# Kernel tuning notes

Hardware: AMD Instinct MI355X
Metric: run time of the kernel (lower is better)

Reference implementation:

```python
import jax, jax.numpy as jnp
import numpy as np

DIM = 2048
NUM_HEADS = 16
HEAD_DIM = DIM // NUM_HEADS
EPS = 1e-6


def rms_norm(x, w, eps=EPS):
    # x: [B, L, C] float; normalize in fp32 semantics
    xf = x.astype(jnp.float32)
    n = xf * jax.lax.rsqrt(jnp.mean(xf * xf, axis=-1, keepdims=True) + eps)
    return n.astype(x.dtype) * w


def rope_apply(x, freqs):
    # x: [B, S, N, D], freqs: [S, D//2]; interleaved rotary in fp32
    xf = x.astype(jnp.float32)
    cos = jnp.cos(freqs).astype(jnp.float32)  # [S, D/2]
    sin = jnp.sin(freqs).astype(jnp.float32)
    B, S, N, D = x.shape
    x2 = xf.reshape(B, S, N, D // 2, 2)
    x_even = x2[..., 0]  # [B,S,N,D/2]
    x_odd = x2[..., 1]
    c = cos[None, :, None, :]
    s = sin[None, :, None, :]
    r_even = x_even * c - x_odd * s
    r_odd = x_even * s + x_odd * c
    out = jnp.stack([r_even, r_odd], axis=-1).reshape(B, S, N, D)
    return out.astype(x.dtype)


def attention(q, k, v):
    # q,k,v: [B, S, N, D] -> [B, S, N, D], standard scaled dot-product
    scale = 1.0 / jnp.sqrt(jnp.asarray(q.shape[-1], q.dtype))
    scores = jnp.einsum('bqnd,bknd->bnqk', q, k) * scale
    p = jax.nn.softmax(scores, axis=-1)
    return jnp.einsum('bnqk,bknd->bqnd', p, v)


def setup_inputs() -> dict:
    key = jax.random.key(0)
    ks = jax.random.split(key, 10)
    B, S = 2, 4096
    x = jax.random.normal(ks[0], (B, S, DIM), dtype=jnp.float32)
    seq_lens = jnp.full((B,), S, dtype=jnp.int32)
    freqs = jax.random.normal(ks[1], (S, HEAD_DIM // 2), dtype=jnp.float32)
    std = 1.0 / np.sqrt(DIM)
    wq = jax.random.normal(ks[2], (DIM, DIM), dtype=jnp.float32) * std
    wk = jax.random.normal(ks[3], (DIM, DIM), dtype=jnp.float32) * std
    wv = jax.random.normal(ks[4], (DIM, DIM), dtype=jnp.float32) * std
    wo = jax.random.normal(ks[5], (DIM, DIM), dtype=jnp.float32) * std
    bq = jnp.zeros((DIM,), jnp.float32)
    bk = jnp.zeros((DIM,), jnp.float32)
    bv = jnp.zeros((DIM,), jnp.float32)
    bo = jnp.zeros((DIM,), jnp.float32)
    gq = jnp.ones((DIM,), jnp.float32)
    gk = jnp.ones((DIM,), jnp.float32)
    return {
        'x': x, 'seq_lens': seq_lens, 'freqs': freqs,
        'wq': wq, 'bq': bq, 'wk': wk, 'bk': bk, 'wv': wv, 'bv': bv,
        'wo': wo, 'bo': bo, 'gq': gq, 'gk': gk,
    }


def reference(x, seq_lens, freqs, wq, bq, wk, bk, wv, bv, wo, bo, gq, gk):
    B, S, C = x.shape
    N, D = NUM_HEADS, HEAD_DIM
    q = rms_norm(x @ wq.T + bq, gq).reshape(B, S, N, D)
    k = rms_norm(x @ wk.T + bk, gk).reshape(B, S, N, D)
    v = (x @ wv.T + bv).reshape(B, S, N, D)
    q = rope_apply(q, freqs)
    k = rope_apply(k, freqs)
    o = attention(q, k, v).reshape(B, S, C)
    return o @ wo.T + bo
```

## Files before the change

kernel.cpp:

```cpp
#include <hip/hip_runtime.h>
#include <hip/hip_bf16.h>

typedef unsigned short u16;
typedef __bf16 bf16x8 __attribute__((ext_vector_type(8)));
typedef float f32x4 __attribute__((ext_vector_type(4)));
typedef float f32x16 __attribute__((ext_vector_type(16)));

#define DIMC  2048
#define NH    16
#define HD    128
#define BSZ   2
#define SEQ   4096
#define MTOK  (BSZ*SEQ)

#define SCALE_L2E (0.08838834764831845f * 1.4426950408889634f)

__device__ __forceinline__ u16 f2bf(float f) {
  unsigned u = __float_as_uint(f);
  u += 0x7fff + ((u >> 16) & 1);
  return (u16)(u >> 16);
}
__device__ __forceinline__ float bf2f(u16 b) {
  return __uint_as_float(((unsigned)b) << 16);
}

__device__ __forceinline__ void gload_lds16(const void* g, void* l) {
  __builtin_amdgcn_global_load_lds(
      (const __attribute__((address_space(1))) void*)g,
      (__attribute__((address_space(3))) void*)l, 16, 0, 0);
}

#define BAR() __builtin_amdgcn_s_barrier()
#define ASM_VMCNT(n) do { asm volatile("s_waitcnt vmcnt(" #n ")" ::: "memory"); \
                          __builtin_amdgcn_sched_barrier(0); } while (0)
#define ASM_LGK0()   do { asm volatile("s_waitcnt lgkmcnt(0)" ::: "memory");    \
                          __builtin_amdgcn_sched_barrier(0); } while (0)

__global__ __launch_bounds__(256) void cast_bf16_k(const float* __restrict__ in,
                                                   u16* __restrict__ out, int n) {
  int i = (blockIdx.x * 256 + threadIdx.x) * 4;
  if (i >= n) return;
  float4 v = *(const float4*)(in + i);
  ushort4 o;
  o.x = f2bf(v.x); o.y = f2bf(v.y); o.z = f2bf(v.z); o.w = f2bf(v.w);
  *(ushort4*)(out + i) = o;
}

__global__ __launch_bounds__(256) void cast_w4_k(
    const float* __restrict__ w0, const float* __restrict__ w1,
    const float* __restrict__ w2, const float* __restrict__ w3,
    u16* __restrict__ out, int n) {
  const int z = blockIdx.z;
  const float* src = (z == 0) ? w0 : (z == 1) ? w1 : (z == 2) ? w2 : w3;
  u16* dst = out + (size_t)z * n;
  int i = (blockIdx.x * 256 + threadIdx.x) * 4;
  if (i >= n) return;
  float4 v = *(const float4*)(src + i);
  ushort4 o;
  o.x = f2bf(v.x); o.y = f2bf(v.y); o.z = f2bf(v.z); o.w = f2bf(v.w);
  *(ushort4*)(dst + i) = o;
}

#define AsBuf(d, h) (SMEM[(d) * 2 + (h)])
#define BsBuf(d, h) (SMEM[4 + (d) * 2 + (h)])

#define STG_A(d, kt, h)                                                        \
  { const u16* s_ = Ag + (size_t)(h) * khalf + (size_t)(kt) * 64;              \
    gload_lds16(s_ + at0, (u16*)AsBuf(d, h) + tid * 8);                        \
    gload_lds16(s_ + at1, (u16*)AsBuf(d, h) + (tid + 512) * 8); }
#define STG_B(d, kt, h)                                                        \
  { const u16* s_ = Bg + (size_t)(h) * khalf + (size_t)(kt) * 64;              \
    gload_lds16(s_ + at0, (u16*)BsBuf(d, h) + tid * 8);                        \
    gload_lds16(s_ + at1, (u16*)BsBuf(d, h) + (tid + 512) * 8); }

#define GPHASE(bb, q, STAGE_CODE, TAIL_CODE)                                   \
  {                                                                            \
    if ((q) == 0) {                                                            \
      _Pragma("unroll") for (int fc = 0; fc < 4; fc++)                         \
        _Pragma("unroll") for (int ks = 0; ks < 2; ks++)                       \
          bfr[fc][ks] = *(const bf16x8*)((const char*)BsBuf(bb, wc >> 1) +     \
              rbB + fc * 2048 + colr[ks]);                                     \
    }                                                                          \
    _Pragma("unroll") for (int e = 0; e < 2; e++)                              \
      _Pragma("unroll") for (int ks = 0; ks < 2; ks++)                         \
        afr[e][ks] = *(const bf16x8*)((const char*)AsBuf(bb, wr) +             \
            rbA + (2 * (q) + e) * 2048 + colr[ks]);                            \
    STAGE_CODE;                                                                \
    BAR();                                                                     \
    ASM_LGK0();                                                                \
    __builtin_amdgcn_s_setprio(1);                                             \
    _Pragma("unroll") for (int e = 0; e < 2; e++)                              \
      _Pragma("unroll") for (int fc = 0; fc < 4; fc++)                         \
        _Pragma("unroll") for (int ks = 0; ks < 2; ks++)                       \
          acc[2 * (q) + e][fc] = __builtin_amdgcn_mfma_f32_16x16x32_bf16(      \
              afr[e][ks], bfr[fc][ks], acc[2 * (q) + e][fc], 0, 0, 0);         \
    __builtin_amdgcn_s_setprio(0);                                             \
    TAIL_CODE;                                                                 \
    BAR();                                                                     \
    __builtin_amdgcn_sched_barrier(0);                                         \
  }

template<bool OUT_F32>
__global__ __launch_bounds__(512, 2) void gemm256_k(
    const u16* __restrict__ A, const u16* __restrict__ Bt,
    const float* __restrict__ b0, const float* __restrict__ b1,
    const float* __restrict__ b2, void* __restrict__ Cout,
    u16* __restrict__ vTout,
    size_t wstride, size_t ostride, int Ndim, int Kdim) {
  __shared__ __align__(16) u16 SMEM[8][128 * 64];
  const int tid = threadIdx.x;
  const int lane = tid & 63, wid = tid >> 6;
  const int wr = wid >> 2, wc = wid & 3;
  const int l15 = lane & 15, lg = lane >> 4;
  const int z = blockIdx.z;

  const u16* W = Bt + (size_t)z * wstride;
  const float* bias = (z == 0) ? b0 : (z == 1 ? b1 : b2);

  const int flat = blockIdx.y * gridDim.x + blockIdx.x;
  const int cpx = (gridDim.x * gridDim.y) >> 3;
  const int swz = (flat & 7) * cpx + (flat >> 3);
  const int bn = (swz % gridDim.x) * 256;
  const int bm = (swz / gridDim.x) * 256;

  const u16* Ag = A + (size_t)bm * Kdim;
  const u16* Bg = W + (size_t)bn * Kdim;
  const size_t khalf = (size_t)128 * Kdim;

  const int r0 = tid >> 3, cc0 = tid & 7;
  const size_t at0 = (size_t)r0 * Kdim + (size_t)((cc0 ^ (r0 & 7)) * 8);
  const size_t at1 = at0 + (size_t)64 * Kdim;

  const int swzl = (l15 & 7) << 4;
  int colr[2];
  colr[0] = (0 * 64 + lg * 16) ^ swzl;
  colr[1] = (1 * 64 + lg * 16) ^ swzl;
  const int rbA = l15 * 128;
  const int rbB = (wc & 1) * 8192 + l15 * 128;

  f32x4 acc[8][4];
#pragma unroll
  for (int i = 0; i < 8; i++)
#pragma unroll
    for (int j = 0; j < 4; j++) acc[i][j] = f32x4{0.f, 0.f, 0.f, 0.f};
  bf16x8 bfr[4][2], afr[2][2];

  STG_A(0, 0, 0); STG_A(0, 0, 1);
  STG_B(0, 0, 0); STG_B(0, 0, 1);
  STG_B(1, 1, 0); STG_B(1, 1, 1);
  ASM_VMCNT(4);
  BAR();

  const int niter = Kdim / 128 - 1;
#pragma unroll 1
  for (int k = 0; k < niter; ++k) {
    const int t = 2 * k;
    GPHASE(0, 0, STG_A(1, t + 1, 0), (void)0);
    GPHASE(0, 1, STG_A(1, t + 1, 1), (void)0);
    GPHASE(0, 2, STG_B(0, t + 2, 0), (void)0);
    GPHASE(0, 3, STG_B(0, t + 2, 1), ASM_VMCNT(4));
    GPHASE(1, 0, STG_A(0, t + 2, 0), (void)0);
    GPHASE(1, 1, STG_A(0, t + 2, 1), (void)0);
    GPHASE(1, 2, STG_B(1, t + 3, 0), (void)0);
    GPHASE(1, 3, STG_B(1, t + 3, 1), ASM_VMCNT(4));
  }
  {
    const int tl = Kdim / 64 - 1;
    GPHASE(0, 0, STG_A(1, tl, 0), (void)0);
    GPHASE(0, 1, STG_A(1, tl, 1), (void)0);
    GPHASE(0, 2, (void)0, (void)0);
    GPHASE(0, 3, (void)0, ASM_VMCNT(0));
    GPHASE(1, 0, (void)0, (void)0);
    GPHASE(1, 1, (void)0, (void)0);
    GPHASE(1, 2, (void)0, (void)0);
    GPHASE(1, 3, (void)0, (void)0);
  }

  if (!OUT_F32 && z == 2) {
    u16* Ts = &SMEM[0][0];
#pragma unroll
    for (int fc = 0; fc < 4; fc++) {
      const int ch = wc * 64 + fc * 16 + l15;
      const float bv = bias[bn + ch];
      const int chx = (ch & 31) << 4;
#pragma unroll
      for (int fr = 0; fr < 8; fr++) {
        const int tok2 = (wr * 128 + fr * 16 + lg * 4) * 2;
        ushort4 w;
        w.x = f2bf(acc[fr][fc][0] + bv);
        w.y = f2bf(acc[fr][fc][1] + bv);
        w.z = f2bf(acc[fr][fc][2] + bv);
        w.w = f2bf(acc[fr][fc][3] + bv);
        *(ushort4*)((char*)Ts + ch * 512 + (tok2 ^ chx)) = w;
      }
    }
    __syncthreads();
    const int b_ = bm >> 12, sm = bm & (SEQ - 1);
    const int l5 = tid & 31, g5 = tid >> 5;
#pragma unroll
    for (int i = 0; i < 16; i++) {
      const int ch = i * 16 + g5;
      const uint4 dv = *(const uint4*)((const char*)Ts + ch * 512 +
                                       ((l5 * 16) ^ ((ch & 31) << 4)));
      *(uint4*)(vTout + (size_t)(b_ * DIMC + bn + ch) * SEQ + sm + l5 * 8) = dv;
    }
  } else {
#pragma unroll
    for (int fc = 0; fc < 4; fc++) {
      const int cj = bn + wc * 64 + fc * 16 + l15;
      const float bv = bias[cj];
#pragma unroll
      for (int fr = 0; fr < 8; fr++) {
        const int row0 = bm + wr * 128 + fr * 16 + lg * 4;
#pragma unroll
        for (int r = 0; r < 4; r++) {
          float v = acc[fr][fc][r] + bv;
          if (OUT_F32)
            ((float*)Cout)[(size_t)z * ostride + (size_t)(row0 + r) * Ndim + cj] = v;
          else
            ((u16*)Cout)[(size_t)z * ostride + (size_t)(row0 + r) * Ndim + cj] = f2bf(v);
        }
      }
    }
  }
}

__global__ __launch_bounds__(256) void rmsrope_k(
    u16* __restrict__ qk, const float* __restrict__ gq, const float* __restrict__ gk,
    const float* __restrict__ freqs) {
  const int t = blockIdx.x;
  const int s = t & (SEQ - 1);
  const int tid = threadIdx.x;
  __shared__ float red[8];

  for (int which = 0; which < 2; ++which) {
    u16* row = qk + (size_t)which * ((size_t)MTOK * DIMC) + (size_t)t * DIMC;
    const float* g = which ? gk : gq;
    const float oscale = which ? 1.0f : SCALE_L2E;
    uint4 raw = *(const uint4*)(row + tid * 8);
    const u16* rb = (const u16*)&raw;
    float v[8], ss = 0.f;
#pragma unroll
    for (int e = 0; e < 8; e++) { v[e] = bf2f(rb[e]); ss += v[e] * v[e]; }
#pragma unroll
    for (int m = 1; m < 64; m <<= 1) ss += __shfl_xor(ss, m);
    if ((tid & 63) == 0) red[which * 4 + (tid >> 6)] = ss;
    __syncthreads();
    float tot = red[which * 4] + red[which * 4 + 1] + red[which * 4 + 2] + red[which * 4 + 3];
    float rms = rsqrtf(tot * (1.0f / (float)DIMC) + 1e-6f);
    const int ch0 = tid * 8;
    const int d0 = ch0 & (HD - 1);
    u16 ob[8];
#pragma unroll
    for (int p = 0; p < 4; p++) {
      float fr = freqs[s * (HD / 2) + (d0 >> 1) + p];
      float cs = cosf(fr), sn = sinf(fr);
      float e = v[2 * p] * rms * g[ch0 + 2 * p];
      float o = v[2 * p + 1] * rms * g[ch0 + 2 * p + 1];
      ob[2 * p]     = f2bf((e * cs - o * sn) * oscale);
      ob[2 * p + 1] = f2bf((e * sn + o * cs) * oscale);
    }
    *(uint4*)(row + tid * 8) = *(const uint4*)ob;
    __syncthreads();
  }
}

#define STAGE(KS, VS, kv0)                                                     \
  _Pragma("unroll") for (int it = 0; it < 4; ++it) {                           \
    const int c = it * 256 + tid;                                              \
    { const int rr = c >> 4, ss = c & 15;                                      \
      gload_lds16(Kp + (size_t)((kv0) + rr) * DIMC + ((ss ^ (rr & 15)) * 8),   \
                  (u16*)(KS) + c * 8); }                                       \
    { const int rr = c >> 3, ss = c & 7;                                       \
      gload_lds16(Vp + (size_t)rr * SEQ + (kv0) + ((ss ^ (rr & 7)) * 8),       \
                  (u16*)(VS) + c * 8); }                                       \
  }

#define CROW(r) (((r) & 3) + 8 * ((r) >> 2) + 4 * hi)

#define COMPUTE(KS, VS)                                                        \
  {                                                                            \
    f32x16 s0, s1;                                                             \
    _Pragma("unroll") for (int i = 0; i < 16; i++) { s0[i] = 0.f; s1[i] = 0.f; } \
    _Pragma("unroll") for (int j = 0; j < 8; ++j) {                            \
      const int byt = (j * 32 + hi * 16);                                      \
      const bf16x8 k0 = *(const bf16x8*)((const char*)(KS) + l31 * 256 +       \
                        (byt ^ ((l31 & 15) << 4)));                            \
      const bf16x8 k1 = *(const bf16x8*)((const char*)(KS) + (32 + l31) * 256 + \
                        (byt ^ ((l31 & 15) << 4)));                            \
      s0 = __builtin_amdgcn_mfma_f32_32x32x16_bf16(k0, qf[j], s0, 0, 0, 0);    \
      s1 = __builtin_amdgcn_mfma_f32_32x32x16_bf16(k1, qf[j], s1, 0, 0, 0);    \
    }                                                                          \
    float rmax = s0[0];                                                        \
    _Pragma("unroll") for (int r = 1; r < 16; r++) rmax = fmaxf(rmax, s0[r]);  \
    _Pragma("unroll") for (int r = 0; r < 16; r++) rmax = fmaxf(rmax, s1[r]);  \
    rmax = fmaxf(rmax, __shfl_xor(rmax, 32));                                  \
    if (!__all(rmax - mq <= 8.0f)) {                                           \
      const float mn = fmaxf(mq, rmax);                                        \
      const float al = exp2f(mq - mn);                                         \
      mq = mn; lq *= al;                                                       \
      _Pragma("unroll") for (int r = 0; r < 16; r++) {                         \
        const float ar = __shfl(al, CROW(r));                                  \
        _Pragma("unroll") for (int d = 0; d < 4; d++) accO[d][r] *= ar;        \
      }                                                                        \
    }                                                                          \
    float p[32]; float rsum = 0.f;                                             \
    _Pragma("unroll") for (int r = 0; r < 16; r++) {                           \
      p[r] = exp2f(s0[r] - mq); rsum += p[r];                                  \
      p[16 + r] = exp2f(s1[r] - mq); rsum += p[16 + r];                        \
    }                                                                          \
    rsum += __shfl_xor(rsum, 32);                                              \
    lq += rsum;                                                                \
    bf16x8 pa[4];                                                              \
    _Pragma("unroll") for (int kb = 0; kb < 2; kb++) {                         \
      unsigned A0, A1, A2, A3, A4, A5, A6, A7;                                 \
      const int bp = kb * 16;                                                  \
      asm("v_cvt_pk_bf16_f32 %0, %1, %2" : "=v"(A0) : "v"(p[bp+0]), "v"(p[bp+1])); \
      asm("v_cvt_pk_bf16_f32 %0, %1, %2" : "=v"(A1) : "v"(p[bp+2]), "v"(p[bp+3])); \
      asm("v_cvt_pk_bf16_f32 %0, %1, %2" : "=v"(A2) : "v"(p[bp+4]), "v"(p[bp+5])); \
      asm("v_cvt_pk_bf16_f32 %0, %1, %2" : "=v"(A3) : "v"(p[bp+6]), "v"(p[bp+7])); \
      asm("v_cvt_pk_bf16_f32 %0, %1, %2" : "=v"(A4) : "v"(p[bp+8]), "v"(p[bp+9])); \
      asm("v_cvt_pk_bf16_f32 %0, %1, %2" : "=v"(A5) : "v"(p[bp+10]), "v"(p[bp+11])); \
      asm("v_cvt_pk_bf16_f32 %0, %1, %2" : "=v"(A6) : "v"(p[bp+12]), "v"(p[bp+13])); \
      asm("v_cvt_pk_bf16_f32 %0, %1, %2" : "=v"(A7) : "v"(p[bp+14]), "v"(p[bp+15])); \
      asm("v_permlane32_swap_b32 %0, %1" : "+v"(A0), "+v"(A2));                \
      asm("v_permlane32_swap_b32 %0, %1" : "+v"(A1), "+v"(A3));                \
      asm("v_permlane32_swap_b32 %0, %1" : "+v"(A4), "+v"(A6));                \
      asm("v_permlane32_swap_b32 %0, %1" : "+v"(A5), "+v"(A7));                \
      union { unsigned u[4]; bf16x8 v; } f0, f1;                               \
      f0.u[0] = A0; f0.u[1] = A1; f0.u[2] = A2; f0.u[3] = A3;                  \
      f1.u[0] = A4; f1.u[1] = A5; f1.u[2] = A6; f1.u[3] = A7;                  \
      pa[kb * 2] = f0.v; pa[kb * 2 + 1] = f1.v;                                \
    }                                                                          \
    _Pragma("unroll") for (int c = 0; c < 4; c++) {                            \
      _Pragma("unroll") for (int d = 0; d < 4; d++) {                          \
        const int vrow = d * 32 + l31;                                         \
        const bf16x8 vb = *(const bf16x8*)((const char*)(VS) + vrow * 128 +    \
                          ((c * 32 + hi * 16) ^ ((vrow & 7) << 4)));           \
        accO[d] = __builtin_amdgcn_mfma_f32_32x32x16_bf16(pa[c], vb, accO[d], 0, 0, 0); \
      }                                                                        \
    }                                                                          \
  }

__global__ __launch_bounds__(256, 2) void attn_k(
    const u16* __restrict__ qbuf, const u16* __restrict__ kbuf,
    const u16* __restrict__ vT, u16* __restrict__ obuf) {
  const int flat = blockIdx.y * gridDim.x + blockIdx.x;
  const int swz = (flat & 7) * 128 + (flat >> 3);
  const int bh = swz >> 5, b = bh >> 4, h = bh & 15;
  const int q0 = (swz & 31) * 128;
  const int tid = threadIdx.x, lane = tid & 63, wid = tid >> 6;
  const int l31 = lane & 31, hi = lane >> 5;

  __shared__ __align__(16) u16 Ks0[64 * 128];
  __shared__ __align__(16) u16 Ks1[64 * 128];
  __shared__ __align__(16) u16 Vs0[128 * 64];
  __shared__ __align__(16) u16 Vs1[128 * 64];

  const size_t qkbase = (size_t)(b * SEQ) * DIMC + h * HD;
  const u16* Qp = qbuf + qkbase;
  const u16* Kp = kbuf + qkbase;
  const u16* Vp = vT + (size_t)(b * DIMC + h * HD) * SEQ;

  bf16x8 qf[8];
  const int qrow = q0 + wid * 32 + l31;
#pragma unroll
  for (int j = 0; j < 8; ++j)
    qf[j] = *(const bf16x8*)(Qp + (size_t)qrow * DIMC + j * 16 + hi * 8);

  float mq = -1e30f, lq = 0.f;
  f32x16 accO[4];
#pragma unroll
  for (int d = 0; d < 4; d++)
#pragma unroll
    for (int i = 0; i < 16; i++) accO[d][i] = 0.f;

  STAGE(Ks0, Vs0, 0);
  __syncthreads();

#pragma unroll 1
  for (int t = 0; t < SEQ / 64; t += 2) {
    STAGE(Ks1, Vs1, (t + 1) * 64);
    COMPUTE(Ks0, Vs0);
    __syncthreads();
    if (t + 2 < SEQ / 64) STAGE(Ks0, Vs0, (t + 2) * 64);
    COMPUTE(Ks1, Vs1);
    __syncthreads();
  }

  const float linv = 1.0f / lq;
  u16* Op = obuf + (size_t)(b * SEQ + q0 + wid * 32) * DIMC + h * HD;
#pragma unroll
  for (int r = 0; r < 16; r++) {
    const float lr = __shfl(linv, CROW(r));
    const int orow = CROW(r);
#pragma unroll
    for (int d = 0; d < 4; d++)
      Op[(size_t)orow * DIMC + d * 32 + l31] = f2bf(accO[d][r] * lr);
  }
}

extern "C" void kernel_launch(void* const* d_in, const int* in_sizes, int n_in,
                              void* d_out, int out_size, void* d_ws, size_t ws_size,
                              hipStream_t stream) {
  const float* x     = (const float*)d_in[0];
  const float* freqs = (const float*)d_in[2];
  const float* wq = (const float*)d_in[3];
  const float* bq = (const float*)d_in[4];
  const float* wk = (const float*)d_in[5];
  const float* bk = (const float*)d_in[6];
  const float* wv = (const float*)d_in[7];
  const float* bv = (const float*)d_in[8];
  const float* wo = (const float*)d_in[9];
  const float* bo = (const float*)d_in[10];
  const float* gq = (const float*)d_in[11];
  const float* gk = (const float*)d_in[12];

  const size_t WS = (size_t)DIMC * DIMC;
  const size_t QS = (size_t)MTOK * DIMC;
  char* ws = (char*)d_ws;
  u16* xb  = (u16*)ws;  ws += QS * 2;
  u16* wb  = (u16*)ws;  ws += 4 * WS * 2;
  u16* qkv = (u16*)ws;  ws += 3 * QS * 2;
  u16* vT  = (u16*)ws;  ws += QS * 2;
  u16* ob  = (u16*)ws;  ws += QS * 2;

  cast_bf16_k<<<(int)(QS / 1024), 256, 0, stream>>>(x, xb, (int)QS);
  cast_w4_k<<<dim3((int)(WS / 1024), 1, 4), 256, 0, stream>>>(wq, wk, wv, wo, wb, (int)WS);

  gemm256_k<false><<<dim3(DIMC / 256, MTOK / 256, 3), 512, 0, stream>>>(
      xb, wb, bq, bk, bv, qkv, vT, WS, QS, DIMC, DIMC);

  rmsrope_k<<<MTOK, 256, 0, stream>>>(qkv, gq, gk, freqs);
  attn_k<<<dim3(SEQ / 128, BSZ * NH), 256, 0, stream>>>(qkv, qkv + 1 * QS, vT, ob);

  gemm256_k<true><<<dim3(DIMC / 256, MTOK / 256, 1), 512, 0, stream>>>(
      ob, wb + 3 * WS, bo, bo, bo, d_out, nullptr, 0, 0, DIMC, DIMC);
}
```

Baseline: 642.9 us.

## Software-pipeline QK^T of next tile with softmax and PV of current tile

```diff
diff --git a/kernel.cpp b/kernel.cpp
--- a/kernel.cpp
+++ b/kernel.cpp
@@ -265,36 +265,44 @@
   }
 }
 
-#define STAGE(KS, VS, kv0)                                                     \
+#define STAGE_K(KS, kv0)                                                       \
   _Pragma("unroll") for (int it = 0; it < 4; ++it) {                           \
     const int c = it * 256 + tid;                                              \
-    { const int rr = c >> 4, ss = c & 15;                                      \
-      gload_lds16(Kp + (size_t)((kv0) + rr) * DIMC + ((ss ^ (rr & 15)) * 8),   \
-                  (u16*)(KS) + c * 8); }                                       \
-    { const int rr = c >> 3, ss = c & 7;                                       \
-      gload_lds16(Vp + (size_t)rr * SEQ + (kv0) + ((ss ^ (rr & 7)) * 8),       \
-                  (u16*)(VS) + c * 8); }                                       \
+    const int rr = c >> 4, ss = c & 15;                                        \
+    gload_lds16(Kp + (size_t)((kv0) + rr) * DIMC + ((ss ^ (rr & 15)) * 8),     \
+                (u16*)(KS) + c * 8);                                           \
+  }
+#define STAGE_V(VS, kv0)                                                       \
+  _Pragma("unroll") for (int it = 0; it < 4; ++it) {                           \
+    const int c = it * 256 + tid;                                              \
+    const int rr = c >> 3, ss = c & 7;                                         \
+    gload_lds16(Vp + (size_t)rr * SEQ + (kv0) + ((ss ^ (rr & 7)) * 8),         \
+                (u16*)(VS) + c * 8);                                           \
   }
 
 #define CROW(r) (((r) & 3) + 8 * ((r) >> 2) + 4 * hi)
 
-#define COMPUTE(KS, VS)                                                        \
+#define QKT(KS, S0, S1)                                                        \
   {                                                                            \
-    f32x16 s0, s1;                                                             \
-    _Pragma("unroll") for (int i = 0; i < 16; i++) { s0[i] = 0.f; s1[i] = 0.f; } \
+    _Pragma("unroll") for (int i = 0; i < 16; i++) { S0[i] = 0.f; S1[i] = 0.f; } \
     _Pragma("unroll") for (int j = 0; j < 8; ++j) {                            \
       const int byt = (j * 32 + hi * 16);                                      \
       const bf16x8 k0 = *(const bf16x8*)((const char*)(KS) + l31 * 256 +       \
                         (byt ^ ((l31 & 15) << 4)));                            \
       const bf16x8 k1 = *(const bf16x8*)((const char*)(KS) + (32 + l31) * 256 + \
                         (byt ^ ((l31 & 15) << 4)));                            \
-      s0 = __builtin_amdgcn_mfma_f32_32x32x16_bf16(k0, qf[j], s0, 0, 0, 0);    \
-      s1 = __builtin_amdgcn_mfma_f32_32x32x16_bf16(k1, qf[j], s1, 0, 0, 0);    \
-    }                                                                          \
-    float rmax = s0[0];                                                        \
-    _Pragma("unroll") for (int r = 1; r < 16; r++) rmax = fmaxf(rmax, s0[r]);  \
-    _Pragma("unroll") for (int r = 0; r < 16; r++) rmax = fmaxf(rmax, s1[r]);  \
-    rmax = fmaxf(rmax, __shfl_xor(rmax, 32));                                  \
+      S0 = __builtin_amdgcn_mfma_f32_32x32x16_bf16(k0, qf[j], S0, 0, 0, 0);    \
+      S1 = __builtin_amdgcn_mfma_f32_32x32x16_bf16(k1, qf[j], S1, 0, 0, 0);    \
+    }                                                                          \
+  }
+
+#define SMPV(S0, S1, VB)                                                       \
+  {                                                                            \
+    float mt[16];                                                              \
+    _Pragma("unroll") for (int r = 0; r < 16; r++) mt[r] = fmaxf(S0[r], S1[r]); \
+    _Pragma("unroll") for (int st = 8; st > 0; st >>= 1)                       \
+      _Pragma("unroll") for (int r = 0; r < st; r++) mt[r] = fmaxf(mt[r], mt[r + st]); \
+    float rmax = fmaxf(mt[0], __shfl_xor(mt[0], 32));                          \
     if (!__all(rmax - mq <= 8.0f)) {                                           \
       const float mn = fmaxf(mq, rmax);                                        \
       const float al = exp2f(mq - mn);                                         \
@@ -306,8 +314,8 @@
     }                                                                          \
     float p[32]; float rsum = 0.f;                                             \
     _Pragma("unroll") for (int r = 0; r < 16; r++) {                           \
-      p[r] = exp2f(s0[r] - mq); rsum += p[r];                                  \
-      p[16 + r] = exp2f(s1[r] - mq); rsum += p[16 + r];                        \
+      p[r] = exp2f(S0[r] - mq); rsum += p[r];                                  \
+      p[16 + r] = exp2f(S1[r] - mq); rsum += p[16 + r];                        \
     }                                                                          \
     rsum += __shfl_xor(rsum, 32);                                              \
     lq += rsum;                                                                \
@@ -335,7 +343,7 @@
     _Pragma("unroll") for (int c = 0; c < 4; c++) {                            \
       _Pragma("unroll") for (int d = 0; d < 4; d++) {                          \
         const int vrow = d * 32 + l31;                                         \
-        const bf16x8 vb = *(const bf16x8*)((const char*)(VS) + vrow * 128 +    \
+        const bf16x8 vb = *(const bf16x8*)((const char*)(VB) + vrow * 128 +    \
                           ((c * 32 + hi * 16) ^ ((vrow & 7) << 4)));           \
         accO[d] = __builtin_amdgcn_mfma_f32_32x32x16_bf16(pa[c], vb, accO[d], 0, 0, 0); \
       }                                                                        \
@@ -356,6 +364,7 @@
   __shared__ __align__(16) u16 Ks1[64 * 128];
   __shared__ __align__(16) u16 Vs0[128 * 64];
   __shared__ __align__(16) u16 Vs1[128 * 64];
+  __shared__ __align__(16) u16 Vs2[128 * 64];
 
   const size_t qkbase = (size_t)(b * SEQ) * DIMC + h * HD;
   const u16* Qp = qbuf + qkbase;
@@ -375,18 +384,33 @@
 #pragma unroll
     for (int i = 0; i < 16; i++) accO[d][i] = 0.f;
 
-  STAGE(Ks0, Vs0, 0);
+  f32x16 sA0, sA1, sB0, sB1;
+  const u16* va = Vs0;
+  const u16* vb2 = Vs1;
+  u16* vc = Vs2;
+
+  STAGE_K(Ks0, 0); STAGE_V(Vs0, 0);
   __syncthreads();
+  QKT(Ks0, sA0, sA1);
+  STAGE_K(Ks1, 64); STAGE_V(Vs1, 64);
+  __syncthreads();
 
 #pragma unroll 1
-  for (int t = 0; t < SEQ / 64; t += 2) {
-    STAGE(Ks1, Vs1, (t + 1) * 64);
-    COMPUTE(Ks0, Vs0);
+  for (int t = 0; t < 62; t += 2) {
+    STAGE_K(Ks0, (t + 2) * 64); STAGE_V(vc, (t + 2) * 64);
+    QKT(Ks1, sB0, sB1);
+    SMPV(sA0, sA1, va);
     __syncthreads();
-    if (t + 2 < SEQ / 64) STAGE(Ks0, Vs0, (t + 2) * 64);
-    COMPUTE(Ks1, Vs1);
+    STAGE_K(Ks1, (t + 3) * 64); STAGE_V((u16*)va, (t + 3) * 64);
+    QKT(Ks0, sA0, sA1);
+    SMPV(sB0, sB1, vb2);
     __syncthreads();
-  }
+    const u16* tmp = va;
+    va = vc; vc = (u16*)vb2; vb2 = tmp;
+  }
+  QKT(Ks1, sB0, sB1);
+  SMPV(sA0, sA1, va);
+  SMPV(sB0, sB1, vb2);
 
   const float linv = 1.0f / lq;
   u16* Op = obuf + (size_t)(b * SEQ + q0 + wid * 32) * DIMC + h * HD;
```

New measurement: 644.0 us. No clear change (+0.2%).
